# Performance work log

Hardware: AMD Instinct MI355X
Metric: run time of the kernel (lower is better)

The kernel has to match this reference:

```python
import jax, jax.numpy as jnp
import numpy as np

E, H, I, K = 8, 1024, 768, 2
T = 2048  # flattened batch*seq tokens

def setup_inputs() -> dict:
    key = jax.random.key(0)
    k1, k2, k3, k4, k5 = jax.random.split(key, 5)
    hidden_states = jax.random.normal(k1, (T, H), dtype=jnp.float32)
    gate_up_proj = jax.random.normal(k2, (E, 2 * I, H), dtype=jnp.float32) * 0.02
    down_proj = jax.random.normal(k3, (E, H, I), dtype=jnp.float32) * 0.02
    top_k_index = jax.random.randint(k4, (T, K), 0, E)
    top_k_weights = jax.nn.softmax(jax.random.normal(k5, (T, K), dtype=jnp.float32), axis=-1)
    return {
        "hidden_states": hidden_states,
        "gate_up_proj": gate_up_proj,
        "down_proj": down_proj,
        "top_k_index": top_k_index,
        "top_k_weights": top_k_weights,
    }


def reference(hidden_states, gate_up_proj, down_proj, top_k_index, top_k_weights):
    # hidden_states: [T, H]; gate_up_proj: [E, 2I, H]; down_proj: [E, H, I]
    # top_k_index: [T, K] int; top_k_weights: [T, K] float
    num_experts = gate_up_proj.shape[0]
    # Combine weights per (token, expert): zero for unrouted experts, so the
    # dense-over-experts compute below yields exactly the routed MoE output.
    onehot = jax.nn.one_hot(top_k_index, num_experts, dtype=hidden_states.dtype)  # [T, K, E]
    combine = jnp.einsum("tke,tk->te", onehot, top_k_weights)  # [T, E]
    # Grouped GEMM 1: fused gate+up projection for all experts.
    gu = jnp.einsum("th,eoh->teo", hidden_states, gate_up_proj)  # [T, E, 2I]
    inter = gu.shape[-1] // 2
    gate, up = gu[..., :inter], gu[..., inter:]
    h = jax.nn.silu(gate) * up  # [T, E, I]
    # Grouped GEMM 2: down projection.
    expert_out = jnp.einsum("tei,ehi->teh", h, down_proj)  # [T, E, H]
    return jnp.einsum("teh,te->th", expert_out, combine)  # [T, H]
```

## Files before the change

### kernel.cpp

```cpp
#include <hip/hip_runtime.h>
#include <hip/hip_bf16.h>

#define T_TOK   2048
#define NEXP    8
#define HDIM    1024
#define IDIM    768
#define TOPK    2
#define NASSIGN (T_TOK*TOPK)
#define MT      64
#define MAX_TILES 72
#define SLOT_PAD 4608

typedef unsigned short u16;
typedef unsigned int   u32;

typedef __bf16 bf16x8 __attribute__((ext_vector_type(8)));
typedef float  f32x4  __attribute__((ext_vector_type(4)));

struct Meta {
  int n_tiles;
  int _pad[15];
  int tile_e[80];
  int tile_m[80];
  int tile_n[80];
};

__device__ __forceinline__ u16 f2bf(float f) {
  u32 x = __float_as_uint(f);
  return (u16)((x + 0x7fffu + ((x >> 16) & 1u)) >> 16);
}

__device__ __forceinline__ int4 pack8(const float* __restrict__ p) {
  float4 a = *(const float4*)p;
  float4 b = *(const float4*)(p + 4);
  union { u16 u[8]; int4 v; } r;
  r.u[0] = f2bf(a.x); r.u[1] = f2bf(a.y); r.u[2] = f2bf(a.z); r.u[3] = f2bf(a.w);
  r.u[4] = f2bf(b.x); r.u[5] = f2bf(b.y); r.u[6] = f2bf(b.z); r.u[7] = f2bf(b.w);
  return r.v;
}

__device__ __forceinline__ bf16x8 asbf(int4 v) {
  return __builtin_bit_cast(bf16x8, v);
}

__device__ __forceinline__ void gll(const void* g, void* l) {
  __builtin_amdgcn_global_load_lds(
      (const __attribute__((address_space(1))) u32*)g,
      (__attribute__((address_space(3))) u32*)l, 16, 0, 0);
}

__global__ __launch_bounds__(256) void prep_k(
    const float* __restrict__ hs, const float* __restrict__ gup,
    const float* __restrict__ down, const int* __restrict__ topk,
    const float* __restrict__ tw,
    u16* __restrict__ hs16, u16* __restrict__ gup16, u16* __restrict__ down16,
    Meta* __restrict__ meta, int* __restrict__ slot_token, float* __restrict__ slot_w,
    float* __restrict__ out) {
  int tid = threadIdx.x;

  if (blockIdx.x == 0) {
    __shared__ int s_cnt[NEXP], s_off[NEXP], s_cur[NEXP];
    if (tid < NEXP) { s_cnt[tid] = 0; s_cur[tid] = 0; }
    __syncthreads();
    for (int i = tid; i < NASSIGN; i += 256)
      atomicAdd(&s_cnt[topk[i]], 1);
    __syncthreads();
    if (tid == 0) {
      int acc = 0, nt = 0;
      for (int e = 0; e < NEXP; ++e) {
        s_off[e] = acc;
        int c = s_cnt[e];
        for (int mb = 0; mb < c; mb += MT) {
          meta->tile_e[nt] = e;
          meta->tile_m[nt] = acc + mb;
          meta->tile_n[nt] = (c - mb) < MT ? (c - mb) : MT;
          ++nt;
        }
        acc += c;
      }
      meta->n_tiles = nt;
    }
    __syncthreads();
    for (int i = tid; i < NASSIGN; i += 256) {
      int e = topk[i];
      int p = s_off[e] + atomicAdd(&s_cur[e], 1);
      slot_token[p] = i / TOPK;
      slot_w[p]     = tw[i];
    }
    for (int i = NASSIGN + tid; i < SLOT_PAD; i += 256) {
      slot_token[i] = 0;
      slot_w[i]     = 0.0f;
    }
  }

  const size_t NG_GUP = (size_t)NEXP * 2 * IDIM * HDIM / 8;
  const size_t NG_DWN = (size_t)NEXP * HDIM * IDIM / 8;
  const size_t NG_HS  = (size_t)T_TOK * HDIM / 8;
  const size_t NG_OUT = (size_t)T_TOK * HDIM / 4;
  const size_t TOT = NG_GUP + NG_DWN + NG_HS + NG_OUT;
  for (size_t g = (size_t)blockIdx.x * 256 + tid; g < TOT; g += (size_t)gridDim.x * 256) {
    if (g < NG_GUP) {
      *(int4*)(gup16 + g * 8) = pack8(gup + g * 8);
    } else if (g < NG_GUP + NG_DWN) {
      size_t i = g - NG_GUP;
      *(int4*)(down16 + i * 8) = pack8(down + i * 8);
    } else if (g < NG_GUP + NG_DWN + NG_HS) {
      size_t i = g - NG_GUP - NG_DWN;
      *(int4*)(hs16 + i * 8) = pack8(hs + i * 8);
    } else {
      size_t i = g - NG_GUP - NG_DWN - NG_HS;
      int4 z = {0, 0, 0, 0};
      *(int4*)(out + i * 4) = z;
    }
  }
}

__global__ __launch_bounds__(256, 3) void gemm1_k(
    const u16* __restrict__ hs16, const u16* __restrict__ gup16,
    const Meta* __restrict__ meta, const int* __restrict__ slot_token,
    const float* __restrict__ slot_w, u16* __restrict__ hbuf) {
  int bid = blockIdx.x;
  int wg = (bid & 7) * 108 + (bid >> 3);
  int tile = wg / 12, y = wg % 12;
  if (tile >= meta->n_tiles) return;
  int e = meta->tile_e[tile], mbase = meta->tile_m[tile], nrows = meta->tile_n[tile];
  int n0 = y * 64;

  __shared__ int4 lds[2][3][512];
  int tid = threadIdx.x, lane = tid & 63, w = tid >> 6, wm = w >> 1, wn = w & 1;
  f32x4 accg[2][2] = {}, accu[2][2] = {};

  const u16* gb = gup16 + (size_t)e * (2 * IDIM) * HDIM + (size_t)n0 * HDIM;
  const u16* ub = gb + (size_t)IDIM * HDIM;

  int c0 = tid, c1 = tid + 256;
  int r0 = c0 >> 3, s0 = (c0 & 7) ^ (r0 & 7);
  int r1 = c1 >> 3, s1 = (c1 & 7) ^ (r1 & 7);
  const u16* a0 = hs16 + (size_t)slot_token[mbase + r0] * HDIM + s0 * 8;
  const u16* a1 = hs16 + (size_t)slot_token[mbase + r1] * HDIM + s1 * 8;
  const u16* g0 = gb + (size_t)r0 * HDIM + s0 * 8;
  const u16* g1 = gb + (size_t)r1 * HDIM + s1 * 8;
  const u16* u0 = ub + (size_t)r0 * HDIM + s0 * 8;
  const u16* u1 = ub + (size_t)r1 * HDIM + s1 * 8;

  auto STAGE = [&](int b, int k0) {
    gll(a0 + k0, &lds[b][0][w * 64]);
    gll(a1 + k0, &lds[b][0][256 + w * 64]);
    gll(g0 + k0, &lds[b][1][w * 64]);
    gll(g1 + k0, &lds[b][1][256 + w * 64]);
    gll(u0 + k0, &lds[b][2][w * 64]);
    gll(u1 + k0, &lds[b][2][256 + w * 64]);
  };

  STAGE(0, 0);
  __syncthreads();
  int cur = 0;
  for (int k0 = 0; k0 < HDIM; k0 += 64) {
    if (k0 + 64 < HDIM) STAGE(cur ^ 1, k0 + 64);
    #pragma unroll
    for (int ks = 0; ks < 2; ++ks) {
      bf16x8 af[2], bgf[2], buf_[2];
      int slot = ks * 4 + (lane >> 4);
      #pragma unroll
      for (int i = 0; i < 2; ++i) {
        int row = wm * 32 + i * 16 + (lane & 15);
        af[i] = asbf(lds[cur][0][(row << 3) | (slot ^ (row & 7))]);
      }
      #pragma unroll
      for (int j = 0; j < 2; ++j) {
        int row = wn * 32 + j * 16 + (lane & 15);
        int idx = (row << 3) | (slot ^ (row & 7));
        bgf[j]  = asbf(lds[cur][1][idx]);
        buf_[j] = asbf(lds[cur][2][idx]);
      }
      #pragma unroll
      for (int i = 0; i < 2; ++i)
        #pragma unroll
        for (int j = 0; j < 2; ++j) {
          accg[i][j] = __builtin_amdgcn_mfma_f32_16x16x32_bf16(af[i], bgf[j],  accg[i][j], 0, 0, 0);
          accu[i][j] = __builtin_amdgcn_mfma_f32_16x16x32_bf16(af[i], buf_[j], accu[i][j], 0, 0, 0);
        }
    }
    __syncthreads();
    cur ^= 1;
  }

  int fq = lane >> 4, fr = lane & 15;
  #pragma unroll
  for (int i = 0; i < 2; ++i)
    #pragma unroll
    for (int r = 0; r < 4; ++r) {
      int row = wm * 32 + i * 16 + fq * 4 + r;
      if (row < nrows) {
        float wgt = slot_w[mbase + row];
        #pragma unroll
        for (int j = 0; j < 2; ++j) {
          float g = accg[i][j][r], u = accu[i][j][r];
          float s = g / (1.0f + __expf(-g));
          hbuf[(size_t)(mbase + row) * IDIM + n0 + wn * 32 + j * 16 + fr] = f2bf(s * u * wgt);
        }
      }
    }
}

__global__ __launch_bounds__(256, 3) void gemm2_k(
    const u16* __restrict__ hbuf, const u16* __restrict__ down16,
    const Meta* __restrict__ meta, const int* __restrict__ slot_token,
    float* __restrict__ out) {
  int bid = blockIdx.x;
  int wg = (bid & 7) * 144 + (bid >> 3);
  int tile = wg / 16, y = wg % 16;
  if (tile >= meta->n_tiles) return;
  int e = meta->tile_e[tile], mbase = meta->tile_m[tile], nrows = meta->tile_n[tile];
  int n0 = y * 64;

  __shared__ int4 lds[2][2][512];
  int tid = threadIdx.x, lane = tid & 63, w = tid >> 6, wm = w >> 1, wn = w & 1;
  f32x4 acc[2][2] = {};
  const u16* db = down16 + (size_t)e * HDIM * IDIM + (size_t)n0 * IDIM;

  int c0 = tid, c1 = tid + 256;
  int r0 = c0 >> 3, s0 = (c0 & 7) ^ (r0 & 7);
  int r1 = c1 >> 3, s1 = (c1 & 7) ^ (r1 & 7);
  const u16* a0 = hbuf + (size_t)(mbase + r0) * IDIM + s0 * 8;
  const u16* a1 = hbuf + (size_t)(mbase + r1) * IDIM + s1 * 8;
  const u16* b0 = db + (size_t)r0 * IDIM + s0 * 8;
  const u16* b1 = db + (size_t)r1 * IDIM + s1 * 8;

  auto STAGE = [&](int b, int k0) {
    gll(a0 + k0, &lds[b][0][w * 64]);
    gll(a1 + k0, &lds[b][0][256 + w * 64]);
    gll(b0 + k0, &lds[b][1][w * 64]);
    gll(b1 + k0, &lds[b][1][256 + w * 64]);
  };

  STAGE(0, 0);
  __syncthreads();
  int cur = 0;
  for (int k0 = 0; k0 < IDIM; k0 += 64) {
    if (k0 + 64 < IDIM) STAGE(cur ^ 1, k0 + 64);
    #pragma unroll
    for (int ks = 0; ks < 2; ++ks) {
      bf16x8 af[2], bf[2];
      int slot = ks * 4 + (lane >> 4);
      #pragma unroll
      for (int i = 0; i < 2; ++i) {
        int row = wm * 32 + i * 16 + (lane & 15);
        af[i] = asbf(lds[cur][0][(row << 3) | (slot ^ (row & 7))]);
      }
      #pragma unroll
      for (int j = 0; j < 2; ++j) {
        int row = wn * 32 + j * 16 + (lane & 15);
        bf[j] = asbf(lds[cur][1][(row << 3) | (slot ^ (row & 7))]);
      }
      #pragma unroll
      for (int i = 0; i < 2; ++i)
        #pragma unroll
        for (int j = 0; j < 2; ++j)
          acc[i][j] = __builtin_amdgcn_mfma_f32_16x16x32_bf16(af[i], bf[j], acc[i][j], 0, 0, 0);
    }
    __syncthreads();
    cur ^= 1;
  }

  int fq = lane >> 4, fr = lane & 15;
  #pragma unroll
  for (int i = 0; i < 2; ++i)
    #pragma unroll
    for (int r = 0; r < 4; ++r) {
      int row = wm * 32 + i * 16 + fq * 4 + r;
      if (row < nrows) {
        int tok = slot_token[mbase + row];
        #pragma unroll
        for (int j = 0; j < 2; ++j)
          atomicAdd(out + (size_t)tok * HDIM + n0 + wn * 32 + j * 16 + fr, acc[i][j][r]);
      }
    }
}

extern "C" void kernel_launch(void* const* d_in, const int* in_sizes, int n_in,
                              void* d_out, int out_size, void* d_ws, size_t ws_size,
                              hipStream_t stream) {
  const float* hs   = (const float*)d_in[0];
  const float* gup  = (const float*)d_in[1];
  const float* down = (const float*)d_in[2];
  const int*   topk = (const int*)d_in[3];
  const float* tw   = (const float*)d_in[4];
  float* out = (float*)d_out;

  const size_t o_hs16   = 65536;
  const size_t o_hbuf   = o_hs16 + (size_t)T_TOK * HDIM * 2;
  const size_t o_gup16  = o_hbuf + (size_t)SLOT_PAD * IDIM * 2;
  const size_t o_down16 = o_gup16 + (size_t)NEXP * 2 * IDIM * HDIM * 2;
  const size_t needed   = o_down16 + (size_t)NEXP * HDIM * IDIM * 2;

  char* ws = (char*)d_ws;
  Meta*  meta       = (Meta*)ws;
  int*   slot_token = (int*)(ws + 4096);
  float* slot_w     = (float*)(ws + 24576);
  u16*   hs16       = (u16*)(ws + o_hs16);
  u16*   hbuf       = (u16*)(ws + o_hbuf);
  u16*   gup16      = (u16*)(ws + o_gup16);
  u16*   down16     = (u16*)(ws + o_down16);

  if (ws_size < needed) return;

  prep_k<<<2048, 256, 0, stream>>>(hs, gup, down, topk, tw,
                                   hs16, gup16, down16, meta, slot_token, slot_w, out);
  gemm1_k<<<MAX_TILES * 12, 256, 0, stream>>>(hs16, gup16, meta, slot_token, slot_w, hbuf);
  gemm2_k<<<MAX_TILES * 16, 256, 0, stream>>>(hbuf, down16, meta, slot_token, out);
}
```

Measured before the change: 198.6 us.

## Triple-buffer GEMM K-loops with vmcnt waits and restructure prep conversion

```diff
diff --git a/kernel.cpp b/kernel.cpp
--- a/kernel.cpp
+++ b/kernel.cpp
@@ -91,31 +91,36 @@
       slot_token[i] = 0;
       slot_w[i]     = 0.0f;
     }
+    return;
   }
 
   const size_t NG_GUP = (size_t)NEXP * 2 * IDIM * HDIM / 8;
   const size_t NG_DWN = (size_t)NEXP * HDIM * IDIM / 8;
   const size_t NG_HS  = (size_t)T_TOK * HDIM / 8;
   const size_t NG_OUT = (size_t)T_TOK * HDIM / 4;
-  const size_t TOT = NG_GUP + NG_DWN + NG_HS + NG_OUT;
-  for (size_t g = (size_t)blockIdx.x * 256 + tid; g < TOT; g += (size_t)gridDim.x * 256) {
-    if (g < NG_GUP) {
-      *(int4*)(gup16 + g * 8) = pack8(gup + g * 8);
-    } else if (g < NG_GUP + NG_DWN) {
-      size_t i = g - NG_GUP;
-      *(int4*)(down16 + i * 8) = pack8(down + i * 8);
-    } else if (g < NG_GUP + NG_DWN + NG_HS) {
-      size_t i = g - NG_GUP - NG_DWN;
-      *(int4*)(hs16 + i * 8) = pack8(hs + i * 8);
-    } else {
-      size_t i = g - NG_GUP - NG_DWN - NG_HS;
-      int4 z = {0, 0, 0, 0};
-      *(int4*)(out + i * 4) = z;
-    }
-  }
-}
-
-__global__ __launch_bounds__(256, 3) void gemm1_k(
+  size_t gid    = ((size_t)(blockIdx.x - 1) * 256 + tid) * 2;
+  size_t stride = (size_t)(gridDim.x - 1) * 256 * 2;
+
+  for (size_t g = gid; g < NG_GUP; g += stride) {
+    *(int4*)(gup16 + g * 8)     = pack8(gup + g * 8);
+    *(int4*)(gup16 + g * 8 + 8) = pack8(gup + g * 8 + 8);
+  }
+  for (size_t g = gid; g < NG_DWN; g += stride) {
+    *(int4*)(down16 + g * 8)     = pack8(down + g * 8);
+    *(int4*)(down16 + g * 8 + 8) = pack8(down + g * 8 + 8);
+  }
+  for (size_t g = gid; g < NG_HS; g += stride) {
+    *(int4*)(hs16 + g * 8)     = pack8(hs + g * 8);
+    *(int4*)(hs16 + g * 8 + 8) = pack8(hs + g * 8 + 8);
+  }
+  int4 z = {0, 0, 0, 0};
+  for (size_t g = gid; g < NG_OUT; g += stride) {
+    *(int4*)(out + g * 4)     = z;
+    *(int4*)(out + g * 4 + 4) = z;
+  }
+}
+
+__global__ __launch_bounds__(256, 2) void gemm1_k(
     const u16* __restrict__ hs16, const u16* __restrict__ gup16,
     const Meta* __restrict__ meta, const int* __restrict__ slot_token,
     const float* __restrict__ slot_w, u16* __restrict__ hbuf) {
@@ -126,7 +131,7 @@
   int e = meta->tile_e[tile], mbase = meta->tile_m[tile], nrows = meta->tile_n[tile];
   int n0 = y * 64;
 
-  __shared__ int4 lds[2][3][512];
+  __shared__ int4 lds[3][3][512];
   int tid = threadIdx.x, lane = tid & 63, w = tid >> 6, wm = w >> 1, wn = w & 1;
   f32x4 accg[2][2] = {}, accu[2][2] = {};
 
@@ -153,10 +158,16 @@
   };
 
   STAGE(0, 0);
-  __syncthreads();
-  int cur = 0;
-  for (int k0 = 0; k0 < HDIM; k0 += 64) {
-    if (k0 + 64 < HDIM) STAGE(cur ^ 1, k0 + 64);
+  STAGE(1, 64);
+  #pragma unroll
+  for (int kt = 0; kt < 16; ++kt) {
+    __builtin_amdgcn_s_barrier();
+    if (kt + 2 < 16) STAGE((kt + 2) % 3, (kt + 2) * 64);
+    if (kt < 14)       asm volatile("s_waitcnt vmcnt(12)" ::: "memory");
+    else if (kt == 14) asm volatile("s_waitcnt vmcnt(6)" ::: "memory");
+    else               asm volatile("s_waitcnt vmcnt(0)" ::: "memory");
+    __builtin_amdgcn_sched_barrier(0);
+    const int cur = kt % 3;
     #pragma unroll
     for (int ks = 0; ks < 2; ++ks) {
       bf16x8 af[2], bgf[2], buf_[2];
@@ -181,8 +192,6 @@
           accu[i][j] = __builtin_amdgcn_mfma_f32_16x16x32_bf16(af[i], buf_[j], accu[i][j], 0, 0, 0);
         }
     }
-    __syncthreads();
-    cur ^= 1;
   }
 
   int fq = lane >> 4, fr = lane & 15;
@@ -214,7 +223,7 @@
   int e = meta->tile_e[tile], mbase = meta->tile_m[tile], nrows = meta->tile_n[tile];
   int n0 = y * 64;
 
-  __shared__ int4 lds[2][2][512];
+  __shared__ int4 lds[3][2][512];
   int tid = threadIdx.x, lane = tid & 63, w = tid >> 6, wm = w >> 1, wn = w & 1;
   f32x4 acc[2][2] = {};
   const u16* db = down16 + (size_t)e * HDIM * IDIM + (size_t)n0 * IDIM;
@@ -235,10 +244,16 @@
   };
 
   STAGE(0, 0);
-  __syncthreads();
-  int cur = 0;
-  for (int k0 = 0; k0 < IDIM; k0 += 64) {
-    if (k0 + 64 < IDIM) STAGE(cur ^ 1, k0 + 64);
+  STAGE(1, 64);
+  #pragma unroll
+  for (int kt = 0; kt < 12; ++kt) {
+    __builtin_amdgcn_s_barrier();
+    if (kt + 2 < 12) STAGE((kt + 2) % 3, (kt + 2) * 64);
+    if (kt < 10)       asm volatile("s_waitcnt vmcnt(8)" ::: "memory");
+    else if (kt == 10) asm volatile("s_waitcnt vmcnt(4)" ::: "memory");
+    else               asm volatile("s_waitcnt vmcnt(0)" ::: "memory");
+    __builtin_amdgcn_sched_barrier(0);
+    const int cur = kt % 3;
     #pragma unroll
     for (int ks = 0; ks < 2; ++ks) {
       bf16x8 af[2], bf[2];
@@ -259,8 +274,6 @@
         for (int j = 0; j < 2; ++j)
           acc[i][j] = __builtin_amdgcn_mfma_f32_16x16x32_bf16(af[i], bf[j], acc[i][j], 0, 0, 0);
     }
-    __syncthreads();
-    cur ^= 1;
   }
 
   int fq = lane >> 4, fr = lane & 15;
@@ -305,7 +318,7 @@
 
   if (ws_size < needed) return;
 
-  prep_k<<<2048, 256, 0, stream>>>(hs, gup, down, topk, tw,
+  prep_k<<<4096, 256, 0, stream>>>(hs, gup, down, topk, tw,
                                    hs16, gup16, down16, meta, slot_token, slot_w, out);
   gemm1_k<<<MAX_TILES * 12, 256, 0, stream>>>(hs16, gup16, meta, slot_token, slot_w, hbuf);
   gemm2_k<<<MAX_TILES * 16, 256, 0, stream>>>(hbuf, down16, meta, slot_token, out);
```

Measured after the change: 178.7 us. 1.11x faster.
